# Kernel tuning notes

Measured on AMD Instinct MI355X. Metric: run time of the kernel, lower is better.

The kernel has to match this reference:

```python
import jax, jax.numpy as jnp
from jax import lax
import numpy as np

EPS = 4e-3            # geoopt float32 ball boundary eps
MAXNORM = 1.0 - EPS   # c = 1 Poincare ball


def _norm(x):
    return jnp.sqrt(jnp.maximum(jnp.sum(x * x, axis=-1, keepdims=True), 1e-15))


def expmap0(u):
    n = _norm(u)
    return jnp.tanh(n) * u / n


def projx(x):
    n = _norm(x)
    return jnp.where(n > MAXNORM, x * (MAXNORM / n), x)


def mobius_add(x, y):
    x2 = jnp.sum(x * x, -1, keepdims=True)
    y2 = jnp.sum(y * y, -1, keepdims=True)
    xy = jnp.sum(x * y, -1, keepdims=True)
    num = (1.0 + 2.0 * xy + y2) * x + (1.0 - x2) * y
    den = 1.0 + 2.0 * xy + x2 * y2
    return num / jnp.maximum(den, 1e-15)


def mamba_layer(x, inW, convW, convb, xpW, dtW, dtb, A_log, Dp, outW):
    # x: [B,T,H]; inW: [2*Din,H]; convW: [Din,K]; xpW: [R+2N,Din]; dtW: [Din,R]
    B, T, H = x.shape
    Din, N = A_log.shape
    K = convW.shape[-1]
    R = dtW.shape[-1]
    xz = jnp.einsum('bth,dh->btd', x, inW)              # [B,T,2*Din]
    xr, z = jnp.split(xz, 2, axis=-1)
    xc = lax.conv_general_dilated(jnp.transpose(xr, (0, 2, 1)), convW[:, None, :],
                                  (1,), [(K - 1, 0)], feature_group_count=Din)
    u = jax.nn.silu(jnp.transpose(xc + convb[None, :, None], (0, 2, 1)))  # [B,T,Din]
    x_dbl = jnp.einsum('btd,ed->bte', u, xpW)           # [B,T,R+2N]
    dt_r, Bm, Cm = x_dbl[..., :R], x_dbl[..., R:R + N], x_dbl[..., R + N:]
    dt = jax.nn.softplus(jnp.einsum('btr,dr->btd', dt_r, dtW) + dtb)      # [B,T,Din]
    A = -jnp.exp(A_log)                                 # [Din,N]
    dA = jnp.exp(dt[..., None] * A)                     # [B,T,Din,N]
    dBu = dt[..., None] * Bm[:, :, None, :] * u[..., None]

    def step(h, ins):
        dA_t, dBu_t, C_t = ins
        h = dA_t * h + dBu_t                            # [B,Din,N]
        return h, jnp.einsum('bdn,bn->bd', h, C_t)

    h0 = jnp.zeros((B, Din, N), x.dtype)
    _, ys = lax.scan(step, h0, (jnp.moveaxis(dA, 1, 0), jnp.moveaxis(dBu, 1, 0), jnp.moveaxis(Cm, 1, 0)))
    y = jnp.moveaxis(ys, 0, 1) + Dp * u                 # [B,T,Din]
    return jnp.einsum('btd,hd->bth', y * jax.nn.silu(z), outW)


def _encode(xs, inp_W, inp_b, in_proj_W, conv_W, conv_b, xproj_W, dt_W, dt_b, A_log, D_skip, out_W, outp_W, outp_b):
    # xs: [4,B,T,1]; params carry leading branch dim 4, then layer dim 3
    def branch(x, iW, ib, ipW, cW, cb, xpW, dW, db, Al, Dp, oW, opW, opb):
        h = jnp.einsum('bti,hi->bth', x, iW) + ib
        for l in range(ipW.shape[0]):
            h = mamba_layer(h, ipW[l], cW[l], cb[l], xpW[l], dW[l], db[l], Al[l], Dp[l], oW[l])
        return jnp.tanh(jnp.einsum('bth,eh->bte', h, opW) + opb)
    return jax.vmap(branch)(xs, inp_W, inp_b, in_proj_W, conv_W, conv_b, xproj_W, dt_W, dt_b, A_log, D_skip, out_W, outp_W, outp_b)


def setup_inputs() -> dict:
    key = jax.random.key(0)
    ks = jax.random.split(key, 24)
    Br, B, T, H, Din, N, K, R, E, L = 4, 32, 1024, 64, 128, 16, 4, 4, 32, 3

    def rn(k, shape, s=0.05):
        return jax.random.normal(k, shape, jnp.float32) * s

    A_init = jnp.log(jnp.arange(1, N + 1, dtype=jnp.float32))
    return {
        'trend': jax.random.normal(ks[0], (B, T, 1), jnp.float32),
        'seasonal_weekly': jax.random.normal(ks[1], (B, T, 1), jnp.float32),
        'seasonal_daily': jax.random.normal(ks[2], (B, T, 1), jnp.float32),
        'residual': jax.random.normal(ks[3], (B, T, 1), jnp.float32),
        'inp_W': rn(ks[4], (Br, H, 1), 0.5),
        'inp_b': rn(ks[5], (Br, H)),
        'in_proj_W': rn(ks[6], (Br, L, 2 * Din, H)),
        'conv_W': rn(ks[7], (Br, L, Din, K), 0.2),
        'conv_b': rn(ks[8], (Br, L, Din)),
        'xproj_W': rn(ks[9], (Br, L, R + 2 * N, Din)),
        'dt_W': rn(ks[10], (Br, L, Din, R), 0.2),
        'dt_b': rn(ks[11], (Br, L, Din), 0.5) - 4.0,  # softplus(dt_b) small
        'A_log': jnp.tile(A_init, (Br, L, Din, 1)) + rn(ks[12], (Br, L, Din, N), 0.01),
        'D_skip': jnp.ones((Br, L, Din), jnp.float32) + rn(ks[13], (Br, L, Din), 0.01),
        'out_W': rn(ks[14], (Br, L, H, Din)),
        'outp_W': rn(ks[15], (Br, E, H)),
        'outp_b': rn(ks[16], (Br, E)),
    }


def reference(trend, seasonal_weekly, seasonal_daily, residual, inp_W, inp_b, in_proj_W, conv_W, conv_b, xproj_W, dt_W, dt_b, A_log, D_skip, out_W, outp_W, outp_b):
    xs = jnp.stack([trend, seasonal_weekly, seasonal_daily, residual], 0)  # [4,B,T,1]
    z = _encode(xs, inp_W, inp_b, in_proj_W, conv_W, conv_b, xproj_W, dt_W, dt_b, A_log, D_skip, out_W, outp_W, outp_b)  # [4,B,T,E]
    zh = projx(expmap0(z))
    t, w, d, r = zh[0], zh[1], zh[2], zh[3]
    comb = projx(mobius_add(mobius_add(t, mobius_add(w, d)), r))
    # stacked [trend_h, weekly_h, daily_h, residual_h, combined_h]
    return jnp.stack([t, w, d, r, comb], 0)
```

## Files before the change

kernel.cpp:

```cpp
#include <hip/hip_runtime.h>
#include <math.h>

#define TT 1024
#define DIN 128
#define HH 64
#define NN 16
#define EE 32
#define LL 3
#define BB 32
#define LOG2E 1.4426950408889634f

__device__ __forceinline__ float siluf(float x) { return x / (1.f + __expf(-x)); }
__device__ __forceinline__ float exp2fast(float x) { return __builtin_amdgcn_exp2f(x); }

typedef __attribute__((ext_vector_type(8))) short bf16x8;
typedef __attribute__((ext_vector_type(4))) float f32x4;

__device__ __forceinline__ void split2(float x, ushort& hi, ushort& lo) {
  unsigned u = __float_as_uint(x);
  hi = (ushort)(u >> 16);
  float rem = x - __uint_as_float((u >> 16) << 16);
  lo = (ushort)(__float_as_uint(rem) >> 16);
}

#define WXZ_N 196608
#define WXD_N 73728
#define WOUT_N 98304

__global__ __launch_bounds__(256) void k_presplit(
    const float* __restrict__ iprojW, const float* __restrict__ xprojW,
    const float* __restrict__ outW,
    ushort* __restrict__ WxzH, ushort* __restrict__ WxzL,
    ushort* __restrict__ WxdH, ushort* __restrict__ WxdL,
    ushort* __restrict__ WoH, ushort* __restrict__ WoL) {
  int idx = blockIdx.x * 256 + threadIdx.x;
  if (idx < WXZ_N) {
    ushort h, l;
    split2(iprojW[idx], h, l);
    WxzH[idx] = h; WxzL[idx] = l;
  }
  if (idx < WXD_N) {
    int k = idx & 127, r = (idx >> 7) % 48, bl = idx / (48 * 128);
    float v = (r < 36) ? xprojW[((size_t)(bl * 36 + r)) * 128 + k] : 0.f;
    ushort h, l;
    split2(v, h, l);
    WxdH[idx] = h; WxdL[idx] = l;
  }
  if (idx < WOUT_N) {
    ushort h, l;
    split2(outW[idx], h, l);
    WoH[idx] = h; WoL[idx] = l;
  }
}

__global__ __launch_bounds__(256) void k_xz(
    const float* __restrict__ x0, const float* __restrict__ x1,
    const float* __restrict__ x2, const float* __restrict__ x3,
    const ushort* __restrict__ WH, const ushort* __restrict__ WL,
    const float* __restrict__ inpW, const float* __restrict__ inpb,
    float* __restrict__ xr, float* __restrict__ zb, int br0) {
  __shared__ __align__(16) ushort Hh[64][72], Hl[64][72];
  const int tid = threadIdx.x;
  const int b  = blockIdx.y;
  const int t0 = blockIdx.x * 64;
  const int br = br0 + (b >> 5);
  {
    const int row = tid >> 2, c0 = (tid & 3) * 16;
    int bb = b & 31;
    const float* xp = (br == 0) ? x0 : (br == 1) ? x1 : (br == 2) ? x2 : x3;
    float xv = xp[bb * TT + t0 + row];
    #pragma unroll
    for (int q = 0; q < 4; ++q) {
      float4 w4 = *(const float4*)(inpW + br * HH + c0 + q * 4);
      float4 b4 = *(const float4*)(inpb + br * HH + c0 + q * 4);
      float4 hv;
      hv.x = xv * w4.x + b4.x; hv.y = xv * w4.y + b4.y;
      hv.z = xv * w4.z + b4.z; hv.w = xv * w4.w + b4.w;
      ushort h0,h1,h2,h3,l0,l1,l2,l3;
      split2(hv.x,h0,l0); split2(hv.y,h1,l1); split2(hv.z,h2,l2); split2(hv.w,h3,l3);
      *(ushort4*)&Hh[row][c0 + q*4] = make_ushort4(h0,h1,h2,h3);
      *(ushort4*)&Hl[row][c0 + q*4] = make_ushort4(l0,l1,l2,l3);
    }
  }
  __syncthreads();
  const int wave = tid >> 6, lane = tid & 63;
  const int quad = lane >> 4, l16 = lane & 15;
  const int nsub = (wave & 1) * 32, tsub = (wave >> 1) * 32;
  const size_t wbase = (size_t)(br * LL) * 256;
  for (int n0 = 0; n0 < 2 * DIN; n0 += 64) {
    f32x4 acc[2][2] = {};
    #pragma unroll
    for (int k0 = 0; k0 < 64; k0 += 32) {
      bf16x8 Ah[2], Al[2], Bh[2], Bl[2];
      #pragma unroll
      for (int i = 0; i < 2; ++i) {
        size_t ro = (wbase + n0 + nsub + i * 16 + l16) * 64 + k0 + quad * 8;
        Ah[i] = *(const bf16x8*)(WH + ro);
        Al[i] = *(const bf16x8*)(WL + ro);
        Bh[i] = *(const bf16x8*)&Hh[tsub + i*16 + l16][k0 + quad*8];
        Bl[i] = *(const bf16x8*)&Hl[tsub + i*16 + l16][k0 + quad*8];
      }
      #pragma unroll
      for (int i = 0; i < 2; ++i)
        #pragma unroll
        for (int j = 0; j < 2; ++j) {
          acc[i][j] = __builtin_amdgcn_mfma_f32_16x16x32_bf16(Ah[i], Bh[j], acc[i][j], 0, 0, 0);
          acc[i][j] = __builtin_amdgcn_mfma_f32_16x16x32_bf16(Ah[i], Bl[j], acc[i][j], 0, 0, 0);
          acc[i][j] = __builtin_amdgcn_mfma_f32_16x16x32_bf16(Al[i], Bh[j], acc[i][j], 0, 0, 0);
        }
    }
    #pragma unroll
    for (int i = 0; i < 2; ++i) {
      #pragma unroll
      for (int r = 0; r < 4; ++r) {
        int n = n0 + nsub + i*16 + quad*4 + r;
        float* dst = (n < DIN) ? (xr + ((size_t)b * DIN + n) * TT)
                               : (zb + ((size_t)b * DIN + (n - DIN)) * TT);
        #pragma unroll
        for (int j = 0; j < 2; ++j)
          dst[t0 + tsub + j*16 + l16] = acc[i][j][r];
      }
    }
  }
}

__global__ __launch_bounds__(256) void k_xds(
    const float* __restrict__ xr, const float* __restrict__ convW,
    const float* __restrict__ convb, const ushort* __restrict__ WH,
    const ushort* __restrict__ WL, const float* __restrict__ dtW,
    const float* __restrict__ dtb, const float* __restrict__ A_log,
    const float* __restrict__ D_skip,
    float* __restrict__ cd, float* __restrict__ Cm,
    float* __restrict__ Hloc, float* __restrict__ g, float* __restrict__ sdt,
    int br0, int l) {
  __shared__ __align__(16) float U[128][66];
  __shared__ __align__(16) float Xs[36][68];
  const int tid = threadIdx.x;
  const int b  = blockIdx.y;
  const int c  = blockIdx.x;
  const int t0 = c * 64;
  const int br = br0 + (b >> 5);
  const int wave = tid >> 6, lane = tid & 63;
  const int quad = lane >> 4, l16 = lane & 15;
  const int tw = wave * 16;
  const size_t wb48 = (size_t)(br * LL + l) * 48 * 128;
  const int dd = tid >> 1, p = tid & 1;
  {
    const int tb = t0 + p * 32;
    const float* src = xr + ((size_t)b * DIN + dd) * TT + tb;
    float r[36];
    #pragma unroll
    for (int q = 0; q < 9; ++q) {
      float4 f = make_float4(0.f, 0.f, 0.f, 0.f);
      if (q > 0 || tb > 0) f = *(const float4*)(src - 4 + q * 4);
      r[q*4+0] = f.x; r[q*4+1] = f.y; r[q*4+2] = f.z; r[q*4+3] = f.w;
    }
    const int wb0 = (br * LL + l) * DIN + dd;
    const float* w = convW + (size_t)wb0 * 4;
    const float w0 = w[0], w1 = w[1], w2 = w[2], w3 = w[3];
    const float cb = convb[wb0];
    #pragma unroll
    for (int i = 0; i < 32; i += 2) {
      float o0 = siluf(r[i+1]*w0 + r[i+2]*w1 + r[i+3]*w2 + r[i+4]*w3 + cb);
      float o1 = siluf(r[i+2]*w0 + r[i+3]*w1 + r[i+4]*w2 + r[i+5]*w3 + cb);
      *(float2*)&U[dd][p * 32 + i] = make_float2(o0, o1);
    }
  }
  __syncthreads();
  f32x4 acc[3] = {};
  #pragma unroll
  for (int k0 = 0; k0 < DIN; k0 += 32) {
    ushort bh[8], bl[8];
    #pragma unroll
    for (int j = 0; j < 8; ++j)
      split2(U[k0 + quad * 8 + j][tw + l16], bh[j], bl[j]);
    bf16x8 Bh = *(bf16x8*)bh, Bl = *(bf16x8*)bl;
    #pragma unroll
    for (int nf = 0; nf < 3; ++nf) {
      size_t ro = wb48 + (size_t)(nf * 16 + l16) * 128 + k0 + quad * 8;
      bf16x8 Whf = *(const bf16x8*)(WH + ro);
      bf16x8 Wlf = *(const bf16x8*)(WL + ro);
      acc[nf] = __builtin_amdgcn_mfma_f32_16x16x32_bf16(Whf, Bh, acc[nf], 0, 0, 0);
      acc[nf] = __builtin_amdgcn_mfma_f32_16x16x32_bf16(Whf, Bl, acc[nf], 0, 0, 0);
      acc[nf] = __builtin_amdgcn_mfma_f32_16x16x32_bf16(Wlf, Bh, acc[nf], 0, 0, 0);
    }
  }
  #pragma unroll
  for (int nf = 0; nf < 3; ++nf) {
    #pragma unroll
    for (int r = 0; r < 4; ++r) {
      int n = nf * 16 + quad * 4 + r;
      if (n < 36) Xs[n][tw + l16] = acc[nf][r];
    }
  }
  __syncthreads();
  {
    int n = tid >> 4, i0 = (tid & 15) * 4;
    *(float4*)(Cm + ((size_t)b * NN + n) * TT + t0 + i0) = *(float4*)&Xs[20 + n][i0];
  }
  const int n0s = p * 8;
  const int wbase = (br * LL + l) * DIN + dd;
  const float* wd = dtW + (size_t)wbase * 4;
  const float w0 = wd[0], w1 = wd[1], w2 = wd[2], w3 = wd[3];
  const float bias = dtb[wbase];
  float Ac[8];
  #pragma unroll
  for (int j = 0; j < 8; ++j)
    Ac[j] = -LOG2E * __expf(A_log[(size_t)wbase * NN + n0s + j]);
  const float Dp = D_skip[wbase];
  float hst[8] = {0.f,0.f,0.f,0.f,0.f,0.f,0.f,0.f};
  float sd = 0.f;
  float* gp  = g  + ((size_t)b * DIN + dd) * TT + t0;
  float* cdp = cd + ((size_t)b * DIN + dd) * TT + t0;
  for (int t8 = 0; t8 < 64; t8 += 8) {
    float4 a0 = *(const float4*)&Xs[0][t8], a0b = *(const float4*)&Xs[0][t8 + 4];
    float4 a1 = *(const float4*)&Xs[1][t8], a1b = *(const float4*)&Xs[1][t8 + 4];
    float4 a2 = *(const float4*)&Xs[2][t8], a2b = *(const float4*)&Xs[2][t8 + 4];
    float4 a3 = *(const float4*)&Xs[3][t8], a3b = *(const float4*)&Xs[3][t8 + 4];
    float x0v[8] = {a0.x,a0.y,a0.z,a0.w,a0b.x,a0b.y,a0b.z,a0b.w};
    float x1v[8] = {a1.x,a1.y,a1.z,a1.w,a1b.x,a1b.y,a1b.z,a1b.w};
    float x2v[8] = {a2.x,a2.y,a2.z,a2.w,a2b.x,a2b.y,a2b.z,a2b.w};
    float x3v[8] = {a3.x,a3.y,a3.z,a3.w,a3b.x,a3b.y,a3b.z,a3b.w};
    float us[8];
    {
      float2 u0 = *(const float2*)&U[dd][t8];
      float2 u1 = *(const float2*)&U[dd][t8 + 2];
      float2 u2 = *(const float2*)&U[dd][t8 + 4];
      float2 u3 = *(const float2*)&U[dd][t8 + 6];
      us[0]=u0.x; us[1]=u0.y; us[2]=u1.x; us[3]=u1.y;
      us[4]=u2.x; us[5]=u2.y; us[6]=u3.x; us[7]=u3.y;
    }
    float dts[8], cds[8], du[8];
    #pragma unroll
    for (int s = 0; s < 8; ++s) {
      float sv = x0v[s]*w0 + x1v[s]*w1 + x2v[s]*w2 + x3v[s]*w3 + bias;
      float e = __expf(-fabsf(sv));
      float dtv = fmaxf(sv, 0.f) + __logf(1.f + e);
      sd += dtv;
      dts[s] = dtv;
      cds[s] = sd;
      du[s] = dtv * us[s];
    }
    float acc8[8] = {0.f,0.f,0.f,0.f,0.f,0.f,0.f,0.f};
    #pragma unroll
    for (int j = 0; j < 8; ++j) {
      int n = n0s + j;
      float4 bq0 = *(const float4*)&Xs[4 + n][t8];
      float4 bq1 = *(const float4*)&Xs[4 + n][t8 + 4];
      float4 cq0 = *(const float4*)&Xs[20 + n][t8];
      float4 cq1 = *(const float4*)&Xs[20 + n][t8 + 4];
      float Bv[8] = {bq0.x,bq0.y,bq0.z,bq0.w,bq1.x,bq1.y,bq1.z,bq1.w};
      float Cv[8] = {cq0.x,cq0.y,cq0.z,cq0.w,cq1.x,cq1.y,cq1.z,cq1.w};
      float hj = hst[j], an = Ac[j];
      #pragma unroll
      for (int s = 0; s < 8; ++s) {
        hj = exp2fast(dts[s] * an) * hj + du[s] * Bv[s];
        acc8[s] += hj * Cv[s];
      }
      hst[j] = hj;
    }
    #pragma unroll
    for (int s = 0; s < 8; ++s) {
      float tot = acc8[s] + __shfl_xor(acc8[s], 1, 2);
      acc8[s] = tot + Dp * us[s];
    }
    if (p == 0) {
      *(float4*)(gp + t8)      = make_float4(acc8[0], acc8[1], acc8[2], acc8[3]);
      *(float4*)(gp + t8 + 4)  = make_float4(acc8[4], acc8[5], acc8[6], acc8[7]);
      *(float4*)(cdp + t8)     = make_float4(cds[0], cds[1], cds[2], cds[3]);
      *(float4*)(cdp + t8 + 4) = make_float4(cds[4], cds[5], cds[6], cds[7]);
    }
  }
  {
    float* hp = Hloc + (((size_t)b * DIN + dd) * 16 + c) * 16 + n0s;
    *(float4*)hp       = make_float4(hst[0], hst[1], hst[2], hst[3]);
    *(float4*)(hp + 4) = make_float4(hst[4], hst[5], hst[6], hst[7]);
  }
  if (p == 0) sdt[((size_t)b * DIN + dd) * 16 + c] = sd;
}

__global__ __launch_bounds__(256) void k_scan2(
    const float* __restrict__ cdc, const float* __restrict__ Cm,
    const float* __restrict__ A_log, const float* __restrict__ Hloc,
    const float* __restrict__ sdt, float* __restrict__ g, int br0, int l) {
  __shared__ __align__(16) float Cl[16][68];
  __shared__ __align__(16) float HinL[32][16];
  const int bx  = blockIdx.x;
  const int b   = bx / 60;
  const int rem = bx % 60;
  const int c   = (rem >> 2) + 1;
  const int dq  = rem & 3;
  const int tid = threadIdx.x;
  const int br  = br0 + (b >> 5);
  {
    int row = tid >> 4, cc = (tid & 15) * 4;
    *(float4*)&Cl[row][cc] = *(const float4*)(Cm + ((size_t)b * NN + row) * TT + c * 64 + cc);
  }
  const int dloc = tid >> 3, tg = tid & 7;
  const int d  = dq * 32 + dloc;
  size_t off = ((size_t)b * DIN + d) * TT + c * 64 + tg * 8;
  float* gp = g + off;
  float4 y0 = *(const float4*)gp;
  float4 y1 = *(const float4*)(gp + 4);
  float4 cq0 = *(const float4*)(cdc + off);
  float4 cq1 = *(const float4*)(cdc + off + 4);
  {
    int n0 = (tid & 7) * 2;
    int wbase = (br * LL + l) * DIN + d;
    float a0 = -LOG2E * __expf(A_log[(size_t)wbase * NN + n0]);
    float a1 = -LOG2E * __expf(A_log[(size_t)wbase * NN + n0 + 1]);
    float h0 = 0.f, h1 = 0.f;
    const float* sp  = sdt + ((size_t)b * DIN + d) * 16;
    const float* hlb = Hloc + ((size_t)b * DIN + d) * 256;
    for (int cc = 0; cc < c; ++cc) {
      float sdv = sp[cc];
      float2 hl = *(const float2*)(hlb + cc * 16 + n0);
      h0 = exp2fast(a0 * sdv) * h0 + hl.x;
      h1 = exp2fast(a1 * sdv) * h1 + hl.y;
    }
    HinL[dloc][n0] = h0;
    HinL[dloc][n0 + 1] = h1;
  }
  __syncthreads();
  float cd8[8] = {cq0.x, cq0.y, cq0.z, cq0.w, cq1.x, cq1.y, cq1.z, cq1.w};
  const float* al = A_log + (size_t)((br * LL + l) * DIN + d) * NN;
  float Ac16[16];
  #pragma unroll
  for (int n = 0; n < 16; ++n) Ac16[n] = -LOG2E * __expf(al[n]);
  float y8[8] = {y0.x, y0.y, y0.z, y0.w, y1.x, y1.y, y1.z, y1.w};
  const int tbase = tg * 8;
  #pragma unroll
  for (int n = 0; n < 16; ++n) {
    float hv = HinL[dloc][n];
    float an = Ac16[n];
    #pragma unroll
    for (int s = 0; s < 8; ++s)
      y8[s] += Cl[n][tbase + s] * exp2fast(an * cd8[s]) * hv;
  }
  *(float4*)gp       = make_float4(y8[0], y8[1], y8[2], y8[3]);
  *(float4*)(gp + 4) = make_float4(y8[4], y8[5], y8[6], y8[7]);
}

__global__ __launch_bounds__(256) void k_outxz(
    const float* __restrict__ graw, float* zb,
    const ushort* __restrict__ WoHp, const ushort* __restrict__ WoLp,
    const ushort* __restrict__ WxHp, const ushort* __restrict__ WxLp,
    float* __restrict__ xr, int br0, int l) {
  __shared__ __align__(16) ushort Bh_[64][72], Bl_[64][72];
  const int tid = threadIdx.x;
  const int b  = blockIdx.y;
  const int t0 = blockIdx.x * 64;
  const int br = br0 + (b >> 5);
  const int wave = tid >> 6, lane = tid & 63;
  const int quad = lane >> 4, l16 = lane & 15;
  const int hsub = (wave & 1) * 32, tsub = (wave >> 1) * 32;
  const size_t wbo = (size_t)(br * LL + l) * 64;
  f32x4 acc[2][2] = {};
  for (int k0 = 0; k0 < DIN; k0 += 64) {
    __syncthreads();
    {
      int row = tid >> 2, c0 = (tid & 3) * 16;
      #pragma unroll
      for (int q = 0; q < 4; ++q) {
        size_t off = ((size_t)b * DIN + k0 + row) * TT + t0 + c0 + q * 4;
        float4 gv = *(const float4*)(graw + off);
        float4 zv = *(const float4*)(zb + off);
        float a0 = gv.x * siluf(zv.x), a1 = gv.y * siluf(zv.y);
        float a2 = gv.z * siluf(zv.z), a3 = gv.w * siluf(zv.w);
        ushort h0,h1,h2,h3,l0,l1,l2,l3;
        split2(a0,h0,l0); split2(a1,h1,l1); split2(a2,h2,l2); split2(a3,h3,l3);
        *(ushort4*)&Bh_[row][c0 + q*4] = make_ushort4(h0,h1,h2,h3);
        *(ushort4*)&Bl_[row][c0 + q*4] = make_ushort4(l0,l1,l2,l3);
      }
    }
    __syncthreads();
    #pragma unroll
    for (int kk = 0; kk < 64; kk += 32) {
      bf16x8 Ahf[2], Alf[2], Bhf[2], Blf[2];
      #pragma unroll
      for (int i = 0; i < 2; ++i) {
        size_t ro = (wbo + hsub + i * 16 + l16) * 128 + k0 + kk + quad * 8;
        Ahf[i] = *(const bf16x8*)(WoHp + ro);
        Alf[i] = *(const bf16x8*)(WoLp + ro);
        Bhf[i] = *(const bf16x8*)&Bh_[tsub + i*16 + l16][kk + quad*8];
        Blf[i] = *(const bf16x8*)&Bl_[tsub + i*16 + l16][kk + quad*8];
      }
      #pragma unroll
      for (int i = 0; i < 2; ++i)
        #pragma unroll
        for (int j = 0; j < 2; ++j) {
          acc[i][j] = __builtin_amdgcn_mfma_f32_16x16x32_bf16(Ahf[i], Bhf[j], acc[i][j], 0, 0, 0);
          acc[i][j] = __builtin_amdgcn_mfma_f32_16x16x32_bf16(Ahf[i], Blf[j], acc[i][j], 0, 0, 0);
          acc[i][j] = __builtin_amdgcn_mfma_f32_16x16x32_bf16(Alf[i], Bhf[j], acc[i][j], 0, 0, 0);
        }
    }
  }
  __syncthreads();
  #pragma unroll
  for (int i = 0; i < 2; ++i) {
    int hh0 = hsub + i*16 + quad*4;
    #pragma unroll
    for (int j = 0; j < 2; ++j) {
      int t = tsub + j*16 + l16;
      ushort h0,h1,h2,h3,l0,l1,l2,l3;
      split2(acc[i][j][0],h0,l0); split2(acc[i][j][1],h1,l1);
      split2(acc[i][j][2],h2,l2); split2(acc[i][j][3],h3,l3);
      *(ushort2*)&Bh_[t][hh0]     = make_ushort2(h0,h1);
      *(ushort2*)&Bh_[t][hh0 + 2] = make_ushort2(h2,h3);
      *(ushort2*)&Bl_[t][hh0]     = make_ushort2(l0,l1);
      *(ushort2*)&Bl_[t][hh0 + 2] = make_ushort2(l2,l3);
    }
  }
  __syncthreads();
  const size_t wbase = (size_t)(br * LL + (l + 1)) * 256;
  const int nsub = hsub;
  for (int n0 = 0; n0 < 2 * DIN; n0 += 64) {
    f32x4 a2[2][2] = {};
    #pragma unroll
    for (int k0 = 0; k0 < 64; k0 += 32) {
      bf16x8 Ah[2], Al[2], Bh[2], Bl[2];
      #pragma unroll
      for (int i = 0; i < 2; ++i) {
        size_t ro = (wbase + n0 + nsub + i * 16 + l16) * 64 + k0 + quad * 8;
        Ah[i] = *(const bf16x8*)(WxHp + ro);
        Al[i] = *(const bf16x8*)(WxLp + ro);
        Bh[i] = *(const bf16x8*)&Bh_[tsub + i*16 + l16][k0 + quad*8];
        Bl[i] = *(const bf16x8*)&Bl_[tsub + i*16 + l16][k0 + quad*8];
      }
      #pragma unroll
      for (int i = 0; i < 2; ++i)
        #pragma unroll
        for (int j = 0; j < 2; ++j) {
          a2[i][j] = __builtin_amdgcn_mfma_f32_16x16x32_bf16(Ah[i], Bh[j], a2[i][j], 0, 0, 0);
          a2[i][j] = __builtin_amdgcn_mfma_f32_16x16x32_bf16(Ah[i], Bl[j], a2[i][j], 0, 0, 0);
          a2[i][j] = __builtin_amdgcn_mfma_f32_16x16x32_bf16(Al[i], Bh[j], a2[i][j], 0, 0, 0);
        }
    }
    #pragma unroll
    for (int i = 0; i < 2; ++i) {
      #pragma unroll
      for (int r = 0; r < 4; ++r) {
        int n = n0 + nsub + i*16 + quad*4 + r;
        float* dst = (n < DIN) ? (xr + ((size_t)b * DIN + n) * TT)
                               : (zb + ((size_t)b * DIN + (n - DIN)) * TT);
        #pragma unroll
        for (int j = 0; j < 2; ++j)
          dst[t0 + tsub + j*16 + l16] = a2[i][j][r];
      }
    }
  }
}

__global__ __launch_bounds__(256) void k_out(
    const float* __restrict__ graw, const float* __restrict__ zb,
    const ushort* __restrict__ WH, const ushort* __restrict__ WL,
    float* __restrict__ h, int br0, int l) {
  __shared__ __align__(16) ushort Bh_[64][72], Bl_[64][72];
  const int tid = threadIdx.x;
  const int b  = blockIdx.y;
  const int t0 = blockIdx.x * 64;
  const int br = br0 + (b >> 5);
  const int wave = tid >> 6, lane = tid & 63;
  const int quad = lane >> 4, l16 = lane & 15;
  const int hsub = (wave & 1) * 32, tsub = (wave >> 1) * 32;
  const size_t wb = (size_t)(br * LL + l) * 64;
  f32x4 acc[2][2] = {};
  for (int k0 = 0; k0 < DIN; k0 += 64) {
    __syncthreads();
    {
      int row = tid >> 2, c0 = (tid & 3) * 16;
      #pragma unroll
      for (int q = 0; q < 4; ++q) {
        size_t off = ((size_t)b * DIN + k0 + row) * TT + t0 + c0 + q * 4;
        float4 gv = *(const float4*)(graw + off);
        float4 zv = *(const float4*)(zb + off);
        float a0 = gv.x * siluf(zv.x), a1 = gv.y * siluf(zv.y);
        float a2 = gv.z * siluf(zv.z), a3 = gv.w * siluf(zv.w);
        ushort h0,h1,h2,h3,l0,l1,l2,l3;
        split2(a0,h0,l0); split2(a1,h1,l1); split2(a2,h2,l2); split2(a3,h3,l3);
        *(ushort4*)&Bh_[row][c0 + q*4] = make_ushort4(h0,h1,h2,h3);
        *(ushort4*)&Bl_[row][c0 + q*4] = make_ushort4(l0,l1,l2,l3);
      }
    }
    __syncthreads();
    #pragma unroll
    for (int kk = 0; kk < 64; kk += 32) {
      bf16x8 Ahf[2], Alf[2], Bhf[2], Blf[2];
      #pragma unroll
      for (int i = 0; i < 2; ++i) {
        size_t ro = (wb + hsub + i * 16 + l16) * 128 + k0 + kk + quad * 8;
        Ahf[i] = *(const bf16x8*)(WH + ro);
        Alf[i] = *(const bf16x8*)(WL + ro);
        Bhf[i] = *(const bf16x8*)&Bh_[tsub + i*16 + l16][kk + quad*8];
        Blf[i] = *(const bf16x8*)&Bl_[tsub + i*16 + l16][kk + quad*8];
      }
      #pragma unroll
      for (int i = 0; i < 2; ++i)
        #pragma unroll
        for (int j = 0; j < 2; ++j) {
          acc[i][j] = __builtin_amdgcn_mfma_f32_16x16x32_bf16(Ahf[i], Bhf[j], acc[i][j], 0, 0, 0);
          acc[i][j] = __builtin_amdgcn_mfma_f32_16x16x32_bf16(Ahf[i], Blf[j], acc[i][j], 0, 0, 0);
          acc[i][j] = __builtin_amdgcn_mfma_f32_16x16x32_bf16(Alf[i], Bhf[j], acc[i][j], 0, 0, 0);
        }
    }
  }
  #pragma unroll
  for (int i = 0; i < 2; ++i) {
    int hh0 = hsub + i*16 + quad*4;
    #pragma unroll
    for (int j = 0; j < 2; ++j) {
      int t = t0 + tsub + j*16 + l16;
      *(f32x4*)(h + ((size_t)b * TT + t) * HH + hh0) = acc[i][j];
    }
  }
}

__global__ __launch_bounds__(256) void k_ze(
    const float* __restrict__ h, const float* __restrict__ outpW,
    const float* __restrict__ outpb, float* __restrict__ ze, int br0) {
  __shared__ __align__(16) float As[16][132];
  __shared__ __align__(16) float Ws[16][36];
  __shared__ __align__(16) float Cs[128][36];
  const int tid = threadIdx.x;
  const int b  = blockIdx.y;
  const int t0 = blockIdx.x * 128;
  const int br = br0 + (b >> 5);
  const float* W = outpW + (size_t)br * EE * HH;
  float acc[4][4] = {};
  const int ti = tid & 31, ni = tid >> 5;
  for (int k0 = 0; k0 < HH; k0 += 16) {
    __syncthreads();
    {
      int i = tid >> 1, kq = (tid & 1) * 8;
      const float* src = h + ((size_t)b * TT + t0 + i) * HH + k0 + kq;
      float4 a0 = *(const float4*)src;
      float4 a1 = *(const float4*)(src + 4);
      As[kq+0][i]=a0.x; As[kq+1][i]=a0.y; As[kq+2][i]=a0.z; As[kq+3][i]=a0.w;
      As[kq+4][i]=a1.x; As[kq+5][i]=a1.y; As[kq+6][i]=a1.z; As[kq+7][i]=a1.w;
    }
    for (int idx = tid; idx < 512; idx += 256) {
      int jj = idx >> 4, kk = idx & 15;
      Ws[kk][jj] = W[(size_t)jj * HH + k0 + kk];
    }
    __syncthreads();
    #pragma unroll
    for (int kk = 0; kk < 16; ++kk) {
      float4 a = *(const float4*)&As[kk][ti * 4];
      float4 w = *(const float4*)&Ws[kk][ni * 4];
      acc[0][0] += a.x*w.x; acc[0][1] += a.x*w.y; acc[0][2] += a.x*w.z; acc[0][3] += a.x*w.w;
      acc[1][0] += a.y*w.x; acc[1][1] += a.y*w.y; acc[1][2] += a.y*w.z; acc[1][3] += a.y*w.w;
      acc[2][0] += a.z*w.x; acc[2][1] += a.z*w.y; acc[2][2] += a.z*w.z; acc[2][3] += a.z*w.w;
      acc[3][0] += a.w*w.x; acc[3][1] += a.w*w.y; acc[3][2] += a.w*w.z; acc[3][3] += a.w*w.w;
    }
  }
  __syncthreads();
  float bj[4];
  #pragma unroll
  for (int c = 0; c < 4; ++c) bj[c] = outpb[br * EE + ni*4 + c];
  #pragma unroll
  for (int r = 0; r < 4; ++r)
    #pragma unroll
    for (int c = 0; c < 4; ++c)
      Cs[ti*4+r][ni*4+c] = tanhf(acc[r][c] + bj[c]);
  __syncthreads();
  int i = tid >> 1, j16 = (tid & 1) * 16;
  float* dst = ze + (((size_t)(br0 * 32 + b)) * TT + t0 + i) * EE + j16;
  #pragma unroll
  for (int q = 0; q < 4; ++q)
    *(float4*)(dst + q*4) = *(float4*)&Cs[i][j16 + q*4];
}

__device__ __forceinline__ void mobius_add32(const float* x, const float* y, float* o) {
  float x2 = 0.f, y2 = 0.f, xy = 0.f;
  #pragma unroll
  for (int i = 0; i < 32; ++i) { x2 += x[i]*x[i]; y2 += y[i]*y[i]; xy += x[i]*y[i]; }
  float ca  = 1.f + 2.f*xy + y2;
  float cb  = 1.f - x2;
  float den = 1.f + 2.f*xy + x2*y2;
  float inv = 1.f / fmaxf(den, 1e-15f);
  #pragma unroll
  for (int i = 0; i < 32; ++i) o[i] = (ca*x[i] + cb*y[i]) * inv;
}

__global__ __launch_bounds__(256) void k_hyper(const float* __restrict__ ze,
                                               float* __restrict__ out) {
  int idx = blockIdx.x * 256 + threadIdx.x;
  int b = idx >> 10, t = idx & 1023;
  float v[4][32];
  #pragma unroll
  for (int br = 0; br < 4; ++br) {
    const float* p = ze + (((size_t)br * BB + b) * TT + t) * EE;
    float s = 0.f;
    #pragma unroll
    for (int e = 0; e < 32; ++e) { v[br][e] = p[e]; s += v[br][e]*v[br][e]; }
    float nr = sqrtf(fmaxf(s, 1e-15f));
    float sc = tanhf(nr) / nr;
    float s2 = 0.f;
    #pragma unroll
    for (int e = 0; e < 32; ++e) { v[br][e] *= sc; s2 += v[br][e]*v[br][e]; }
    float n2 = sqrtf(fmaxf(s2, 1e-15f));
    if (n2 > 0.996f) {
      float sc2 = 0.996f / n2;
      #pragma unroll
      for (int e = 0; e < 32; ++e) v[br][e] *= sc2;
    }
    float* o = out + (((size_t)br * BB + b) * TT + t) * EE;
    #pragma unroll
    for (int e = 0; e < 32; ++e) o[e] = v[br][e];
  }
  float m1[32], m2[32];
  mobius_add32(v[1], v[2], m1);
  mobius_add32(v[0], m1, m2);
  mobius_add32(m2, v[3], m1);
  float s = 0.f;
  #pragma unroll
  for (int e = 0; e < 32; ++e) s += m1[e]*m1[e];
  float n = sqrtf(fmaxf(s, 1e-15f));
  if (n > 0.996f) {
    float sc = 0.996f / n;
    #pragma unroll
    for (int e = 0; e < 32; ++e) m1[e] *= sc;
  }
  float* o = out + (((size_t)4 * BB + b) * TT + t) * EE;
  #pragma unroll
  for (int e = 0; e < 32; ++e) o[e] = m1[e];
}

extern "C" void kernel_launch(void* const* d_in, const int* in_sizes, int n_in,
                              void* d_out, int out_size, void* d_ws, size_t ws_size,
                              hipStream_t stream) {
  const float* xs0 = (const float*)d_in[0];
  const float* xs1 = (const float*)d_in[1];
  const float* xs2 = (const float*)d_in[2];
  const float* xs3 = (const float*)d_in[3];
  const float* inpW   = (const float*)d_in[4];
  const float* inpb   = (const float*)d_in[5];
  const float* iprojW = (const float*)d_in[6];
  const float* convW  = (const float*)d_in[7];
  const float* convb  = (const float*)d_in[8];
  const float* xprojW = (const float*)d_in[9];
  const float* dtW    = (const float*)d_in[10];
  const float* dtb    = (const float*)d_in[11];
  const float* A_log  = (const float*)d_in[12];
  const float* D_skip = (const float*)d_in[13];
  const float* outW   = (const float*)d_in[14];
  const float* outpW  = (const float*)d_in[15];
  const float* outpb  = (const float*)d_in[16];
  float* out = (float*)d_out;

  const size_t wUshorts = 2 * (WXZ_N + WXD_N + WOUT_N);
  ushort* WxzH = (ushort*)d_ws;
  ushort* WxzL = WxzH + WXZ_N;
  ushort* WxdH = WxzL + WXZ_N;
  ushort* WxdL = WxdH + WXD_N;
  ushort* WoH  = WxdL + WXD_N;
  ushort* WoL  = WoH + WOUT_N;
  float* ws = (float*)(WoL + WOUT_N);

  const size_t zeF = (size_t)4 * BB * TT * EE;
  const size_t perBl = 65536 + 4 * 131072 + 16384 + 2048;
  auto needBytes = [&](int NB) {
    return (zeF + (size_t)NB * 32 * perBl) * 4 + wUshorts * 2;
  };
  int NB = 4;
  if (needBytes(4) > ws_size) NB = 2;
  if (NB == 2 && needBytes(2) > ws_size) NB = 1;
  const int nbl = NB * 32;

  float* ze = ws;
  float* h  = ze + zeF;
  float* xr = h  + (size_t)nbl * 65536;
  float* zb = xr + (size_t)nbl * 131072;
  float* g  = zb + (size_t)nbl * 131072;
  float* cd = g  + (size_t)nbl * 131072;
  float* Cm = cd + (size_t)nbl * 131072;
  float* sdt = Cm + (size_t)nbl * 16384;
  float* Hloc = h;

  k_presplit<<<WXZ_N / 256, 256, 0, stream>>>(iprojW, xprojW, outW,
                                              WxzH, WxzL, WxdH, WxdL, WoH, WoL);

  for (int br0 = 0; br0 < 4; br0 += NB) {
    k_xz<<<dim3(16, nbl), 256, 0, stream>>>(xs0, xs1, xs2, xs3,
                                            WxzH, WxzL, inpW, inpb, xr, zb, br0);
    for (int l = 0; l < LL; ++l) {
      k_xds<<<dim3(16, nbl), 256, 0, stream>>>(xr, convW, convb, WxdH, WxdL,
                                               dtW, dtb, A_log, D_skip,
                                               cd, Cm, Hloc, g, sdt, br0, l);
      k_scan2<<<nbl * 60, 256, 0, stream>>>(cd, Cm, A_log, Hloc, sdt, g, br0, l);
      if (l < LL - 1)
        k_outxz<<<dim3(16, nbl), 256, 0, stream>>>(g, zb, WoH, WoL, WxzH, WxzL,
                                                   xr, br0, l);
      else
        k_out<<<dim3(16, nbl), 256, 0, stream>>>(g, zb, WoH, WoL, h, br0, l);
    }
    k_ze<<<dim3(8, nbl), 256, 0, stream>>>(h, outpW, outpb, ze, br0);
  }
  k_hyper<<<BB * TT / 256, 256, 0, stream>>>(ze, out);
}
```

Before: 935.0 us.

## Double k_xds threads to split state dimension four ways per channel

Raises k_xds from 256 to 512 threads, so each channel is handled by four lanes that each own 4 SSM states instead of two lanes owning 8. The MFMA projection is split so four waves compute the first 32 output rows and the other four compute the last rows. The goal is more parallelism and less serial work per thread in the chunk-local scan. In exchange, the softplus/dt computation is duplicated across more lanes, an extra shuffle stage is added to the reduction, and the MFMA split between wave groups is uneven.

```diff
diff --git a/kernel.cpp b/kernel.cpp
--- a/kernel.cpp
+++ b/kernel.cpp
@@ -124,7 +124,7 @@
   }
 }
 
-__global__ __launch_bounds__(256) void k_xds(
+__global__ __launch_bounds__(512) void k_xds(
     const float* __restrict__ xr, const float* __restrict__ convW,
     const float* __restrict__ convb, const ushort* __restrict__ WH,
     const ushort* __restrict__ WL, const float* __restrict__ dtW,
@@ -142,15 +142,16 @@
   const int br = br0 + (b >> 5);
   const int wave = tid >> 6, lane = tid & 63;
   const int quad = lane >> 4, l16 = lane & 15;
-  const int tw = wave * 16;
+  const int tw  = (wave & 3) * 16;
+  const int nfg = wave >> 2;
   const size_t wb48 = (size_t)(br * LL + l) * 48 * 128;
-  const int dd = tid >> 1, p = tid & 1;
+  const int dd = tid >> 2, p4 = tid & 3;
   {
-    const int tb = t0 + p * 32;
+    const int tb = t0 + p4 * 16;
     const float* src = xr + ((size_t)b * DIN + dd) * TT + tb;
-    float r[36];
-    #pragma unroll
-    for (int q = 0; q < 9; ++q) {
+    float r[20];
+    #pragma unroll
+    for (int q = 0; q < 5; ++q) {
       float4 f = make_float4(0.f, 0.f, 0.f, 0.f);
       if (q > 0 || tb > 0) f = *(const float4*)(src - 4 + q * 4);
       r[q*4+0] = f.x; r[q*4+1] = f.y; r[q*4+2] = f.z; r[q*4+3] = f.w;
@@ -160,14 +161,14 @@
     const float w0 = w[0], w1 = w[1], w2 = w[2], w3 = w[3];
     const float cb = convb[wb0];
     #pragma unroll
-    for (int i = 0; i < 32; i += 2) {
+    for (int i = 0; i < 16; i += 2) {
       float o0 = siluf(r[i+1]*w0 + r[i+2]*w1 + r[i+3]*w2 + r[i+4]*w3 + cb);
       float o1 = siluf(r[i+2]*w0 + r[i+3]*w1 + r[i+4]*w2 + r[i+5]*w3 + cb);
-      *(float2*)&U[dd][p * 32 + i] = make_float2(o0, o1);
+      *(float2*)&U[dd][p4 * 16 + i] = make_float2(o0, o1);
     }
   }
   __syncthreads();
-  f32x4 acc[3] = {};
+  f32x4 acc0 = {}, acc1 = {};
   #pragma unroll
   for (int k0 = 0; k0 < DIN; k0 += 32) {
     ushort bh[8], bl[8];
@@ -175,40 +176,54 @@
     for (int j = 0; j < 8; ++j)
       split2(U[k0 + quad * 8 + j][tw + l16], bh[j], bl[j]);
     bf16x8 Bh = *(bf16x8*)bh, Bl = *(bf16x8*)bl;
-    #pragma unroll
-    for (int nf = 0; nf < 3; ++nf) {
-      size_t ro = wb48 + (size_t)(nf * 16 + l16) * 128 + k0 + quad * 8;
-      bf16x8 Whf = *(const bf16x8*)(WH + ro);
-      bf16x8 Wlf = *(const bf16x8*)(WL + ro);
-      acc[nf] = __builtin_amdgcn_mfma_f32_16x16x32_bf16(Whf, Bh, acc[nf], 0, 0, 0);
-      acc[nf] = __builtin_amdgcn_mfma_f32_16x16x32_bf16(Whf, Bl, acc[nf], 0, 0, 0);
-      acc[nf] = __builtin_amdgcn_mfma_f32_16x16x32_bf16(Wlf, Bh, acc[nf], 0, 0, 0);
-    }
-  }
-  #pragma unroll
-  for (int nf = 0; nf < 3; ++nf) {
+    if (nfg == 0) {
+      size_t ro0 = wb48 + (size_t)(l16) * 128 + k0 + quad * 8;
+      size_t ro1 = wb48 + (size_t)(16 + l16) * 128 + k0 + quad * 8;
+      bf16x8 Wh0 = *(const bf16x8*)(WH + ro0), Wl0 = *(const bf16x8*)(WL + ro0);
+      bf16x8 Wh1 = *(const bf16x8*)(WH + ro1), Wl1 = *(const bf16x8*)(WL + ro1);
+      acc0 = __builtin_amdgcn_mfma_f32_16x16x32_bf16(Wh0, Bh, acc0, 0, 0, 0);
+      acc0 = __builtin_amdgcn_mfma_f32_16x16x32_bf16(Wh0, Bl, acc0, 0, 0, 0);
+      acc0 = __builtin_amdgcn_mfma_f32_16x16x32_bf16(Wl0, Bh, acc0, 0, 0, 0);
+      acc1 = __builtin_amdgcn_mfma_f32_16x16x32_bf16(Wh1, Bh, acc1, 0, 0, 0);
+      acc1 = __builtin_amdgcn_mfma_f32_16x16x32_bf16(Wh1, Bl, acc1, 0, 0, 0);
+      acc1 = __builtin_amdgcn_mfma_f32_16x16x32_bf16(Wl1, Bh, acc1, 0, 0, 0);
+    } else {
+      size_t ro2 = wb48 + (size_t)(32 + l16) * 128 + k0 + quad * 8;
+      bf16x8 Wh2 = *(const bf16x8*)(WH + ro2), Wl2 = *(const bf16x8*)(WL + ro2);
+      acc0 = __builtin_amdgcn_mfma_f32_16x16x32_bf16(Wh2, Bh, acc0, 0, 0, 0);
+      acc0 = __builtin_amdgcn_mfma_f32_16x16x32_bf16(Wh2, Bl, acc0, 0, 0, 0);
+      acc0 = __builtin_amdgcn_mfma_f32_16x16x32_bf16(Wl2, Bh, acc0, 0, 0, 0);
+    }
+  }
+  if (nfg == 0) {
     #pragma unroll
     for (int r = 0; r < 4; ++r) {
-      int n = nf * 16 + quad * 4 + r;
-      if (n < 36) Xs[n][tw + l16] = acc[nf][r];
+      Xs[quad * 4 + r][tw + l16]      = acc0[r];
+      Xs[16 + quad * 4 + r][tw + l16] = acc1[r];
+    }
+  } else {
+    #pragma unroll
+    for (int r = 0; r < 4; ++r) {
+      int n = 32 + quad * 4 + r;
+      if (n < 36) Xs[n][tw + l16] = acc0[r];
     }
   }
   __syncthreads();
-  {
+  if (tid < 256) {
     int n = tid >> 4, i0 = (tid & 15) * 4;
     *(float4*)(Cm + ((size_t)b * NN + n) * TT + t0 + i0) = *(float4*)&Xs[20 + n][i0];
   }
-  const int n0s = p * 8;
+  const int n0s = p4 * 4;
   const int wbase = (br * LL + l) * DIN + dd;
   const float* wd = dtW + (size_t)wbase * 4;
   const float w0 = wd[0], w1 = wd[1], w2 = wd[2], w3 = wd[3];
   const float bias = dtb[wbase];
-  float Ac[8];
-  #pragma unroll
-  for (int j = 0; j < 8; ++j)
+  float Ac[4];
+  #pragma unroll
+  for (int j = 0; j < 4; ++j)
     Ac[j] = -LOG2E * __expf(A_log[(size_t)wbase * NN + n0s + j]);
   const float Dp = D_skip[wbase];
-  float hst[8] = {0.f,0.f,0.f,0.f,0.f,0.f,0.f,0.f};
+  float hst[4] = {0.f,0.f,0.f,0.f};
   float sd = 0.f;
   float* gp  = g  + ((size_t)b * DIN + dd) * TT + t0;
   float* cdp = cd + ((size_t)b * DIN + dd) * TT + t0;
@@ -243,7 +258,7 @@
     }
     float acc8[8] = {0.f,0.f,0.f,0.f,0.f,0.f,0.f,0.f};
     #pragma unroll
-    for (int j = 0; j < 8; ++j) {
+    for (int j = 0; j < 4; ++j) {
       int n = n0s + j;
       float4 bq0 = *(const float4*)&Xs[4 + n][t8];
       float4 bq1 = *(const float4*)&Xs[4 + n][t8 + 4];
@@ -261,10 +276,11 @@
     }
     #pragma unroll
     for (int s = 0; s < 8; ++s) {
-      float tot = acc8[s] + __shfl_xor(acc8[s], 1, 2);
+      float t1  = acc8[s] + __shfl_xor(acc8[s], 1, 4);
+      float tot = t1 + __shfl_xor(t1, 2, 4);
       acc8[s] = tot + Dp * us[s];
     }
-    if (p == 0) {
+    if (p4 == 0) {
       *(float4*)(gp + t8)      = make_float4(acc8[0], acc8[1], acc8[2], acc8[3]);
       *(float4*)(gp + t8 + 4)  = make_float4(acc8[4], acc8[5], acc8[6], acc8[7]);
       *(float4*)(cdp + t8)     = make_float4(cds[0], cds[1], cds[2], cds[3]);
@@ -273,10 +289,9 @@
   }
   {
     float* hp = Hloc + (((size_t)b * DIN + dd) * 16 + c) * 16 + n0s;
-    *(float4*)hp       = make_float4(hst[0], hst[1], hst[2], hst[3]);
-    *(float4*)(hp + 4) = make_float4(hst[4], hst[5], hst[6], hst[7]);
-  }
-  if (p == 0) sdt[((size_t)b * DIN + dd) * 16 + c] = sd;
+    *(float4*)hp = make_float4(hst[0], hst[1], hst[2], hst[3]);
+  }
+  if (p4 == 0) sdt[((size_t)b * DIN + dd) * 16 + c] = sd;
 }
 
 __global__ __launch_bounds__(256) void k_scan2(
@@ -684,7 +699,7 @@
     k_xz<<<dim3(16, nbl), 256, 0, stream>>>(xs0, xs1, xs2, xs3,
                                             WxzH, WxzL, inpW, inpb, xr, zb, br0);
     for (int l = 0; l < LL; ++l) {
-      k_xds<<<dim3(16, nbl), 256, 0, stream>>>(xr, convW, convb, WxdH, WxdL,
+      k_xds<<<dim3(16, nbl), 512, 0, stream>>>(xr, convW, convb, WxdH, WxdL,
                                                dtW, dtb, A_log, D_skip,
                                                cd, Cm, Hloc, g, sdt, br0, l);
       k_scan2<<<nbl * 60, 256, 0, stream>>>(cd, Cm, A_log, Hloc, sdt, g, br0, l);
```

Measured after the change: 973.5 us. 1.04x slower.
